# Kernel optimization log

Hardware: AMD Instinct MI355X
Metric: run time of the kernel (lower is better)

Reference implementation:

```python
import jax, jax.numpy as jnp
import numpy as np

N, M, K = 8192, 100000, 4096


def setup_inputs() -> dict:
    key = jax.random.key(0)
    k0, k1, k2, k3, k4, k5 = jax.random.split(key, 6)
    origins = jax.random.uniform(k0, (N, 2), dtype=jnp.float32)
    directions = jax.random.uniform(k1, (N, 2), dtype=jnp.float32)
    embeddings = jax.random.uniform(k2, (M, 4), dtype=jnp.float32)
    # Cholesky factors: lower-triangular with strictly positive diagonal
    # (mirrors Encoder.update_parameters: tril + abs(diag)+eps)
    L = jnp.tril(jax.random.uniform(k3, (M, 4, 4), dtype=jnp.float32) * 0.1)
    i4 = jnp.arange(4)
    diag = jnp.abs(L[:, i4, i4]) + 1e-2
    chol = L.at[:, i4, i4].set(diag)
    # labels_embedding in {-1, +1} (Encoder maps 0 -> -1)
    labels = jnp.where(jax.random.randint(k4, (M,), 0, 2) == 0, -1.0, 1.0).astype(jnp.float32)
    idx = jax.random.randint(k5, (K,), 0, M, dtype=jnp.int32)
    return {"origins": origins, "directions": directions, "embeddings": embeddings,
            "chol": chol, "labels": labels, "idx": idx}


def reference(origins, directions, embeddings, chol, labels, idx):
    # Encoder: gather selected gaussians, Sigma = L @ L^T
    mu = embeddings[idx]                                   # [K,4]
    Lsel = chol[idx]                                       # [K,4,4]
    Sigma = jnp.einsum('kij,klj->kil', Lsel, Lsel)         # [K,4,4]
    lab = labels[idx]                                      # [K]
    # Decoder: batched 4x4 inverse + quadratic form + exp + sum + sigmoid
    Sigma_inv = jnp.linalg.inv(Sigma)                      # [K,4,4]
    pos = jnp.concatenate([origins, directions], axis=1)   # [N,4]
    diffs = pos[:, None, :] - mu[None, :, :]               # [N,K,4]
    q = jnp.einsum('nkd,kde,nke->nk', diffs, Sigma_inv, diffs)  # [N,K]
    pdf = lab[None, :] * jnp.exp(-0.5 * q)                 # [N,K]
    prob = jax.nn.sigmoid(jnp.sum(pdf, axis=1))            # [N]
    return prob.reshape(-1, 1)
```

## Files before the change

### kernel.cpp

```cpp
#include <hip/hip_runtime.h>
#include <math.h>

#define K_TOTAL 4096
#define N_RAYS  8192
#define S_CHUNKS 128
#define CHUNK (K_TOTAL / S_CHUNKS)
#define R 4
#define BLOCK 256
#define RAYS_PER_BLOCK (BLOCK * R)
#define NGROUPS (N_RAYS / RAYS_PER_BLOCK)

__global__ __launch_bounds__(256, 4) void fused_main_kernel(
    const float* __restrict__ origins,
    const float* __restrict__ directions,
    const float* __restrict__ embeddings,
    const float* __restrict__ chol,
    const float* __restrict__ labels,
    const int*   __restrict__ idx,
    float*       __restrict__ partial)
{
    __shared__ float4 stab[CHUNK * 4];

    int tid = threadIdx.x;
    int s   = blockIdx.y;

    if (tid < CHUNK) {
        int k = s * CHUNK + tid;
        int i = idx[k];

        const float* Lp = chol + (size_t)i * 16;
        float l00 = Lp[0];
        float l10 = Lp[4],  l11 = Lp[5];
        float l20 = Lp[8],  l21 = Lp[9],  l22 = Lp[10];
        float l30 = Lp[12], l31 = Lp[13], l32 = Lp[14], l33 = Lp[15];

        float u0 = 1.0f / l00, u1 = 1.0f / l11, u2 = 1.0f / l22, u3 = 1.0f / l33;

        float m00 = u0;
        float m10 = -u1 * (l10 * m00);
        float m11 = u1;
        float m20 = -u2 * (l20 * m00 + l21 * m10);
        float m21 = -u2 * (l21 * m11);
        float m22 = u2;
        float m30 = -u3 * (l30 * m00 + l31 * m10 + l32 * m20);
        float m31 = -u3 * (l31 * m11 + l32 * m21);
        float m32 = -u3 * (l32 * m22);
        float m33 = u3;

        const float SC = 0.84932180381996511548f;
        m00 *= SC; m10 *= SC; m11 *= SC; m20 *= SC; m21 *= SC;
        m22 *= SC; m30 *= SC; m31 *= SC; m32 *= SC; m33 *= SC;

        float4 mu = *(const float4*)(embeddings + (size_t)i * 4);
        float b0 = -(m00 * mu.x);
        float b1 = -(m10 * mu.x + m11 * mu.y);
        float b2 = -(m20 * mu.x + m21 * mu.y + m22 * mu.z);
        float b3 = -(m30 * mu.x + m31 * mu.y + m32 * mu.z + m33 * mu.w);

        float lab = labels[i];

        stab[tid*4 + 0] = make_float4(m00, m10, m11, m20);
        stab[tid*4 + 1] = make_float4(m21, m22, m30, m31);
        stab[tid*4 + 2] = make_float4(m32, m33, b0, b1);
        stab[tid*4 + 3] = make_float4(b2, b3, lab, 0.0f);
    }

    int base = blockIdx.x * RAYS_PER_BLOCK + tid;

    float p0[R], p1[R], p2[R], p3[R], acc[R];
    #pragma unroll
    for (int r = 0; r < R; ++r) {
        int n = base + r * BLOCK;
        float2 o = ((const float2*)origins)[n];
        float2 d = ((const float2*)directions)[n];
        p0[r] = o.x; p1[r] = o.y; p2[r] = d.x; p3[r] = d.y;
        acc[r] = 0.0f;
    }

    __syncthreads();

    #pragma unroll 8
    for (int k = 0; k < CHUNK; ++k) {
        float4 t0 = stab[k*4 + 0];
        float4 t1 = stab[k*4 + 1];
        float4 t2 = stab[k*4 + 2];
        float4 t3 = stab[k*4 + 3];
        #pragma unroll
        for (int r = 0; r < R; ++r) {
            float y0 = fmaf(t0.x, p0[r], t2.z);
            float y1 = fmaf(t0.z, p1[r], fmaf(t0.y, p0[r], t2.w));
            float y2 = fmaf(t1.y, p2[r], fmaf(t1.x, p1[r], fmaf(t0.w, p0[r], t3.x)));
            float y3 = fmaf(t2.y, p3[r], fmaf(t2.x, p2[r], fmaf(t1.w, p1[r], fmaf(t1.z, p0[r], t3.y))));
            float sq = y0 * y0;
            sq = fmaf(y1, y1, sq);
            sq = fmaf(y2, y2, sq);
            sq = fmaf(y3, y3, sq);
            acc[r] = fmaf(t3.z, __builtin_amdgcn_exp2f(-sq), acc[r]);
        }
    }

    #pragma unroll
    for (int r = 0; r < R; ++r)
        partial[(size_t)s * N_RAYS + base + r * BLOCK] = acc[r];
}

__global__ __launch_bounds__(64) void finish_kernel(
    const float* __restrict__ partial,
    float*       __restrict__ out)
{
    int n = blockIdx.x * 64 + threadIdx.x;
    float v[S_CHUNKS];
    #pragma unroll
    for (int s = 0; s < S_CHUNKS; ++s)
        v[s] = partial[(size_t)s * N_RAYS + n];
    #pragma unroll
    for (int w = S_CHUNKS / 2; w >= 1; w >>= 1)
        #pragma unroll
        for (int s = 0; s < w; ++s)
            v[s] += v[s + w];
    const float L2E = 1.44269504088896340736f;
    out[n] = 1.0f / (1.0f + __builtin_amdgcn_exp2f(-v[0] * L2E));
}

extern "C" void kernel_launch(void* const* d_in, const int* in_sizes, int n_in,
                              void* d_out, int out_size, void* d_ws, size_t ws_size,
                              hipStream_t stream) {
    const float* origins    = (const float*)d_in[0];
    const float* directions = (const float*)d_in[1];
    const float* embeddings = (const float*)d_in[2];
    const float* chol       = (const float*)d_in[3];
    const float* labels     = (const float*)d_in[4];
    const int*   idx        = (const int*)d_in[5];
    float* out = (float*)d_out;

    float* partial = (float*)d_ws;

    fused_main_kernel<<<dim3(NGROUPS, S_CHUNKS), dim3(BLOCK), 0, stream>>>(
        origins, directions, embeddings, chol, labels, idx, partial);

    finish_kernel<<<dim3(N_RAYS / 64), dim3(64), 0, stream>>>(partial, out);
}
```

Before: 86.98 us.

## Precompute Gaussian table in separate kernel and read it via scalar loads

```diff
diff --git a/kernel.cpp b/kernel.cpp
--- a/kernel.cpp
+++ b/kernel.cpp
@@ -10,60 +10,63 @@
 #define RAYS_PER_BLOCK (BLOCK * R)
 #define NGROUPS (N_RAYS / RAYS_PER_BLOCK)
 
-__global__ __launch_bounds__(256, 4) void fused_main_kernel(
-    const float* __restrict__ origins,
-    const float* __restrict__ directions,
+__global__ __launch_bounds__(256) void table_kernel(
     const float* __restrict__ embeddings,
     const float* __restrict__ chol,
     const float* __restrict__ labels,
     const int*   __restrict__ idx,
+    float*       __restrict__ tab)
+{
+    int k = blockIdx.x * 256 + threadIdx.x;
+    if (k >= K_TOTAL) return;
+    int i = idx[k];
+
+    const float* Lp = chol + (size_t)i * 16;
+    float l00 = Lp[0];
+    float l10 = Lp[4],  l11 = Lp[5];
+    float l20 = Lp[8],  l21 = Lp[9],  l22 = Lp[10];
+    float l30 = Lp[12], l31 = Lp[13], l32 = Lp[14], l33 = Lp[15];
+
+    float u0 = 1.0f / l00, u1 = 1.0f / l11, u2 = 1.0f / l22, u3 = 1.0f / l33;
+
+    float m00 = u0;
+    float m10 = -u1 * (l10 * m00);
+    float m11 = u1;
+    float m20 = -u2 * (l20 * m00 + l21 * m10);
+    float m21 = -u2 * (l21 * m11);
+    float m22 = u2;
+    float m30 = -u3 * (l30 * m00 + l31 * m10 + l32 * m20);
+    float m31 = -u3 * (l31 * m11 + l32 * m21);
+    float m32 = -u3 * (l32 * m22);
+    float m33 = u3;
+
+    const float SC = 0.84932180381996511548f;
+    m00 *= SC; m10 *= SC; m11 *= SC; m20 *= SC; m21 *= SC;
+    m22 *= SC; m30 *= SC; m31 *= SC; m32 *= SC; m33 *= SC;
+
+    float4 mu = *(const float4*)(embeddings + (size_t)i * 4);
+    float b0 = -(m00 * mu.x);
+    float b1 = -(m10 * mu.x + m11 * mu.y);
+    float b2 = -(m20 * mu.x + m21 * mu.y + m22 * mu.z);
+    float b3 = -(m30 * mu.x + m31 * mu.y + m32 * mu.z + m33 * mu.w);
+
+    float lab = labels[i];
+
+    float4* t = (float4*)(tab + (size_t)k * 16);
+    t[0] = make_float4(m00, m10, m11, m20);
+    t[1] = make_float4(m21, m22, m30, m31);
+    t[2] = make_float4(m32, m33, b0, b1);
+    t[3] = make_float4(b2, b3, lab, 0.0f);
+}
+
+__global__ __launch_bounds__(256, 4) void fused_main_kernel(
+    const float* __restrict__ origins,
+    const float* __restrict__ directions,
+    const float* __restrict__ tab,
     float*       __restrict__ partial)
 {
-    __shared__ float4 stab[CHUNK * 4];
-
     int tid = threadIdx.x;
     int s   = blockIdx.y;
-
-    if (tid < CHUNK) {
-        int k = s * CHUNK + tid;
-        int i = idx[k];
-
-        const float* Lp = chol + (size_t)i * 16;
-        float l00 = Lp[0];
-        float l10 = Lp[4],  l11 = Lp[5];
-        float l20 = Lp[8],  l21 = Lp[9],  l22 = Lp[10];
-        float l30 = Lp[12], l31 = Lp[13], l32 = Lp[14], l33 = Lp[15];
-
-        float u0 = 1.0f / l00, u1 = 1.0f / l11, u2 = 1.0f / l22, u3 = 1.0f / l33;
-
-        float m00 = u0;
-        float m10 = -u1 * (l10 * m00);
-        float m11 = u1;
-        float m20 = -u2 * (l20 * m00 + l21 * m10);
-        float m21 = -u2 * (l21 * m11);
-        float m22 = u2;
-        float m30 = -u3 * (l30 * m00 + l31 * m10 + l32 * m20);
-        float m31 = -u3 * (l31 * m11 + l32 * m21);
-        float m32 = -u3 * (l32 * m22);
-        float m33 = u3;
-
-        const float SC = 0.84932180381996511548f;
-        m00 *= SC; m10 *= SC; m11 *= SC; m20 *= SC; m21 *= SC;
-        m22 *= SC; m30 *= SC; m31 *= SC; m32 *= SC; m33 *= SC;
-
-        float4 mu = *(const float4*)(embeddings + (size_t)i * 4);
-        float b0 = -(m00 * mu.x);
-        float b1 = -(m10 * mu.x + m11 * mu.y);
-        float b2 = -(m20 * mu.x + m21 * mu.y + m22 * mu.z);
-        float b3 = -(m30 * mu.x + m31 * mu.y + m32 * mu.z + m33 * mu.w);
-
-        float lab = labels[i];
-
-        stab[tid*4 + 0] = make_float4(m00, m10, m11, m20);
-        stab[tid*4 + 1] = make_float4(m21, m22, m30, m31);
-        stab[tid*4 + 2] = make_float4(m32, m33, b0, b1);
-        stab[tid*4 + 3] = make_float4(b2, b3, lab, 0.0f);
-    }
 
     int base = blockIdx.x * RAYS_PER_BLOCK + tid;
 
@@ -77,25 +80,26 @@
         acc[r] = 0.0f;
     }
 
-    __syncthreads();
+    const float* __restrict__ tb = tab + (size_t)s * CHUNK * 16;
 
-    #pragma unroll 8
+    #pragma unroll 2
     for (int k = 0; k < CHUNK; ++k) {
-        float4 t0 = stab[k*4 + 0];
-        float4 t1 = stab[k*4 + 1];
-        float4 t2 = stab[k*4 + 2];
-        float4 t3 = stab[k*4 + 3];
+        const float* t = tb + k * 16;
+        float m00 = t[0],  m10 = t[1],  m11 = t[2],  m20 = t[3];
+        float m21 = t[4],  m22 = t[5],  m30 = t[6],  m31 = t[7];
+        float m32 = t[8],  m33 = t[9],  b0  = t[10], b1  = t[11];
+        float b2  = t[12], b3  = t[13], lab = t[14];
         #pragma unroll
         for (int r = 0; r < R; ++r) {
-            float y0 = fmaf(t0.x, p0[r], t2.z);
-            float y1 = fmaf(t0.z, p1[r], fmaf(t0.y, p0[r], t2.w));
-            float y2 = fmaf(t1.y, p2[r], fmaf(t1.x, p1[r], fmaf(t0.w, p0[r], t3.x)));
-            float y3 = fmaf(t2.y, p3[r], fmaf(t2.x, p2[r], fmaf(t1.w, p1[r], fmaf(t1.z, p0[r], t3.y))));
+            float y0 = fmaf(m00, p0[r], b0);
+            float y1 = fmaf(m11, p1[r], fmaf(m10, p0[r], b1));
+            float y2 = fmaf(m22, p2[r], fmaf(m21, p1[r], fmaf(m20, p0[r], b2)));
+            float y3 = fmaf(m33, p3[r], fmaf(m32, p2[r], fmaf(m31, p1[r], fmaf(m30, p0[r], b3))));
             float sq = y0 * y0;
             sq = fmaf(y1, y1, sq);
             sq = fmaf(y2, y2, sq);
             sq = fmaf(y3, y3, sq);
-            acc[r] = fmaf(t3.z, __builtin_amdgcn_exp2f(-sq), acc[r]);
+            acc[r] = fmaf(lab, __builtin_amdgcn_exp2f(-sq), acc[r]);
         }
     }
 
@@ -134,9 +138,13 @@
     float* out = (float*)d_out;
 
     float* partial = (float*)d_ws;
+    float* tab     = (float*)((char*)d_ws + (size_t)S_CHUNKS * N_RAYS * sizeof(float));
+
+    table_kernel<<<dim3(K_TOTAL / 256), dim3(256), 0, stream>>>(
+        embeddings, chol, labels, idx, tab);
 
     fused_main_kernel<<<dim3(NGROUPS, S_CHUNKS), dim3(BLOCK), 0, stream>>>(
-        origins, directions, embeddings, chol, labels, idx, partial);
+        origins, directions, tab, partial);
 
     finish_kernel<<<dim3(N_RAYS / 64), dim3(64), 0, stream>>>(partial, out);
 }
```

Result: slower. 92.43 us (+6.3%).
